# Performance work log

Measured on AMD Instinct MI355X. Metric: run time of the kernel, lower is better.

The kernel has to match this reference:

```python
import jax, jax.numpy as jnp
import numpy as np

N, E, C, H, EDGE_DIM, HID = 50000, 800000, 128, 8, 64, 512
D = C // H  # head dim = out_channels_conv


def layer_norm(x, g, b, eps=1e-5):
    mu = x.mean(-1, keepdims=True)
    var = ((x - mu) ** 2).mean(-1, keepdims=True)
    return (x - mu) * jax.lax.rsqrt(var + eps) * g + b


def _lin_init(k, fan_in, fan_out):
    s = 1.0 / np.sqrt(fan_in)
    kw, kb = jax.random.split(k)
    w = jax.random.uniform(kw, (fan_in, fan_out), minval=-s, maxval=s, dtype=jnp.float32)
    b = jax.random.uniform(kb, (fan_out,), minval=-s, maxval=s, dtype=jnp.float32)
    return w, b


def setup_inputs() -> dict:
    key = jax.random.key(0)
    ks = jax.random.split(key, 16)
    wq, bq = _lin_init(ks[0], C, C)
    wk, bk = _lin_init(ks[1], C, C)
    wv, bv = _lin_init(ks[2], C, C)
    ws, bs = _lin_init(ks[3], C, C)          # lin_self
    we, be = _lin_init(ks[4], EDGE_DIM, C)   # lin_edge
    wp, bp = _lin_init(ks[5], C, C)          # projection
    w1, b1 = _lin_init(ks[6], C, HID)        # node_dst_mlp[0]
    w2, b2 = _lin_init(ks[7], HID, C)        # node_dst_mlp[2]
    x = jax.random.normal(ks[8], (N, C), dtype=jnp.float32)
    edge_attr = jax.random.normal(ks[9], (E, EDGE_DIM), dtype=jnp.float32)
    edge_index = jax.random.randint(ks[10], (2, E), 0, N, dtype=jnp.int64)
    return dict(
        x=x, edge_attr=edge_attr, edge_index=edge_index,
        wq=wq, bq=bq, wk=wk, bk=bk, wv=wv, bv=bv, ws=ws, bs=bs,
        we=we, be=be, wp=wp, bp=bp, w1=w1, b1=b1, w2=w2, b2=b2,
        ln1_g=jnp.ones((C,), jnp.float32), ln1_b=jnp.zeros((C,), jnp.float32),
        ln2_g=jnp.ones((C,), jnp.float32), ln2_b=jnp.zeros((C,), jnp.float32),
    )


def reference(x, edge_attr, edge_index,
              wq, bq, wk, bk, wv, bv, ws, bs, we, be, wp, bp,
              w1, b1, w2, b2, ln1_g, ln1_b, ln2_g, ln2_b):
    src, dst = edge_index[0], edge_index[1]

    x_skip = x
    xn = layer_norm(x, ln1_g, ln1_b)                       # layer_norm_attention
    x_r = xn @ ws + bs                                     # lin_self residual
    q = (xn @ wq + bq).reshape(N, H, D)
    k = (xn @ wk + bk).reshape(N, H, D)
    v = (xn @ wv + bv).reshape(N, H, D)
    e = (edge_attr @ we + be).reshape(E, H, D)             # lin_edge (edge_pre_mlp = Identity)

    # edge-indexed multi-head attention: softmax over incoming edges per dst node
    ke = k[src] + e                                        # [E,H,D]
    alpha = jnp.einsum('ehd,ehd->eh', q[dst], ke) / np.sqrt(D)   # [E,H]
    amax = jax.lax.stop_gradient(jax.ops.segment_max(alpha, dst, num_segments=N))
    ex = jnp.exp(alpha - amax[dst])
    den = jax.ops.segment_sum(ex, dst, num_segments=N)
    w = ex / (den[dst] + 1e-16)                            # [E,H]
    out = jax.ops.segment_sum(w[:, :, None] * (v[src] + e), dst, num_segments=N)  # [N,H,D]
    out = out.reshape(N, C)

    out = (out + x_r) @ wp + bp                            # projection
    out = out + x_skip
    h = layer_norm(out, ln2_g, ln2_b)                      # layer_norm_mlp_dst
    h = jax.nn.gelu(h @ w1 + b1) @ w2 + b2                 # node_dst_mlp
    nodes_new = out + h
    return nodes_new, edge_attr
```

## Files before the change

kernel.cpp:

```cpp
#include <hip/hip_runtime.h>
#include <hip/hip_bf16.h>
#include <cstdio>

#define NN 50000
#define NE 800000
#define CC 128
#define EDIM 64
#define HIDN 512

using bf16 = __hip_bfloat16;
typedef short sh8 __attribute__((ext_vector_type(8)));
typedef float f32x4 __attribute__((ext_vector_type(4)));

static __device__ __forceinline__ float b2f(bf16 v){ return __bfloat162float(v); }
static __device__ __forceinline__ bf16 f2b(float v){ return __float2bfloat16(v); }
static __device__ __forceinline__ float u2f(unsigned short u){
    union { unsigned int i; float f; } w; w.i = ((unsigned int)u) << 16; return w.f;
}
static __device__ __forceinline__ unsigned short f2u(float f){
    bf16 b = __float2bfloat16(f);
    return *reinterpret_cast<unsigned short*>(&b);
}
static __device__ __forceinline__ float2 loadbf2(const bf16* p){
    __hip_bfloat162 v = *reinterpret_cast<const __hip_bfloat162*>(p);
    return make_float2(__bfloat162float(v.x), __bfloat162float(v.y));
}
static __device__ __forceinline__ float gelu_tanh(float x){
    const float c = 0.7978845608028654f;
    float u = c * (x + 0.044715f * x * x * x);
    return x / (1.0f + __expf(-2.0f * u));
}

constexpr size_t AL(size_t x){ return (x + 255) & ~(size_t)255; }
constexpr size_t OFF_FLAG = 0;
constexpr size_t OFF_DEG  = 256;
constexpr size_t OFF_ROW  = AL(OFF_DEG + (size_t)(NN + 1) * 4);
constexpr size_t OFF_CUR  = AL(OFF_ROW + (size_t)(NN + 1) * 4);
constexpr size_t OFF_EPOS = AL(OFF_CUR + (size_t)NN * 4);
constexpr size_t OFF_SRC  = AL(OFF_EPOS + (size_t)NE * 4);
constexpr size_t OFF_DST  = AL(OFF_SRC + (size_t)NE * 4);
constexpr size_t OFF_QC   = AL(OFF_DST + (size_t)NE * 4);
constexpr size_t OFF_KC   = AL(OFF_QC  + (size_t)NN * CC * 2);
constexpr size_t OFF_VC   = AL(OFF_KC  + (size_t)NN * CC * 2);
constexpr size_t OFF_ATT  = AL(OFF_VC  + (size_t)NN * CC * 2);
constexpr size_t OFF_PRM  = AL(OFF_ATT + (size_t)NN * CC * 2);
constexpr size_t PRM_ELEMS = 4*(16384+128) + 8192+128 + 16384+128 + 65536+512 + 65536+128 + 4*128;
constexpr size_t OFF_ALP  = AL(OFF_PRM + PRM_ELEMS * 2);
constexpr size_t OFF_VP   = AL(OFF_ALP + (size_t)NE * 8 * 4);
constexpr size_t OFF_XRC  = AL(OFF_VP + (size_t)NE * CC * 2);
constexpr size_t OFF_WFQ  = AL(OFF_XRC + (size_t)NN * CC * 2);
constexpr size_t OFF_WFK  = OFF_WFQ + 32768;
constexpr size_t OFF_WFV  = OFF_WFK + 32768;
constexpr size_t OFF_WFS  = OFF_WFV + 32768;
constexpr size_t OFF_WFP  = OFF_WFS + 32768;
constexpr size_t OFF_WF1  = OFF_WFP + 32768;
constexpr size_t OFF_WF2  = OFF_WF1 + 131072;
constexpr size_t OFF_WFE  = OFF_WF2 + 131072;
constexpr size_t OFF_BSUM = OFF_WFE + 16384;
constexpr size_t WS_NEED  = OFF_BSUM + 256;

__global__ void k_detect(const unsigned short* xw, const unsigned int* ew, int* flags){
    __shared__ int sw, sz;
    if (threadIdx.x == 0){ sw = 0; sz = 0; }
    __syncthreads();
    int w = 0;
    for (int i = threadIdx.x; i < 8192; i += 256){
        unsigned e = (xw[i] >> 7) & 0xFF;
        if (e == 0xFF || (e != 0 && (e < 0x60 || e > 0x90))) w++;
    }
    atomicAdd(&sw, w);
    int z = 0;
    for (int i = threadIdx.x; i < 2048; i += 256)
        if (ew[2*i+1] == 0u) z++;
    atomicAdd(&sz, z);
    __syncthreads();
    if (threadIdx.x == 0){
        flags[0] = (sw > 2048) ? 1 : 0;
        flags[1] = (sz > 1536) ? 1 : 0;
    }
}

struct CvtJob { const void* s; bf16* d; int n; };
struct CvtJobs { CvtJob j[20]; };
__global__ void k_cvt_all(CvtJobs jobs, const int* flags){
    const int f = flags[0];
    const int e = blockIdx.x >> 5;
    const CvtJob J = jobs.j[e];
    const int stride = 32 * 256;
    for (int i = (blockIdx.x & 31) * 256 + threadIdx.x; i < J.n; i += stride){
        if (f) J.d[i] = f2b(((const float*)J.s)[i]);
        else   J.d[i] = ((const bf16*)J.s)[i];
    }
}

__global__ void k_cvt_idx(const int* e32, int* srcI, int* dstI, int* deg, const int* flags){
    const int f = flags[1];
    int i = blockIdx.x * blockDim.x + threadIdx.x;
    const int stride = gridDim.x * blockDim.x;
    if (f){
        const long long* e64 = (const long long*)e32;
        for (; i < NE; i += stride){
            srcI[i] = (int)e64[i];
            const int d = (int)e64[NE + i];
            dstI[i] = d;
            atomicAdd(&deg[d], 1);
        }
    } else {
        for (; i < NE; i += stride){
            srcI[i] = e32[i];
            const int d = e32[NE + i];
            dstI[i] = d;
            atomicAdd(&deg[d], 1);
        }
    }
}

struct WJob { const bf16* W; bf16* WF; int K; int N; };
struct WJobs { WJob j[8]; };
__global__ void k_wprep_all(WJobs jobs){
    const WJob J = jobs.j[blockIdx.x / 48];
    const int KS = J.K >> 5;
    const int total = J.K * J.N;
    for (int o = (blockIdx.x % 48) * 256 + threadIdx.x; o < total; o += 48 * 256){
        const int j  = o & 7;
        const int ln = (o >> 3) & 63;
        const int tt = o >> 9;
        const int ks = tt % KS, ct = tt / KS;
        const int kk = (ks << 5) + ((ln >> 4) << 3) + j;
        const int c  = (ct << 4) + (ln & 15);
        J.WF[o] = J.W[kk * J.N + c];
    }
}

#define ASWZ(row, chunk)  (((row) << 8)  + ((((chunk) ^ ((row) & 15))) << 4))
#define HSWZ(row, chunk)  (((row) << 10) + ((((chunk) ^ ((row) & 15))) << 4))
#define EASWZ(row, chunk) (((row) << 7)  + ((((chunk) ^ ((row) & 7)))  << 4))

static __device__ __forceinline__ void gemm_nodes_128(
    const unsigned short* Abase, int row0, int lane,
    const bf16* __restrict__ WF, const bf16* __restrict__ bias,
    bf16* __restrict__ outp, int n0)
{
    const int rA = row0 + (lane & 15);
    sh8 af[4];
    #pragma unroll
    for (int ks = 0; ks < 4; ++ks)
        af[ks] = *(const sh8*)((const char*)Abase + ASWZ(rA, (ks << 2) + (lane >> 4)));
    f32x4 acc[8] = {};
    #pragma unroll
    for (int ks = 0; ks < 4; ++ks)
        #pragma unroll
        for (int ct = 0; ct < 8; ++ct){
            sh8 bfr = *(const sh8*)(WF + ((size_t)((ct << 2) + ks) * 64 + lane) * 8);
            acc[ct] = __builtin_amdgcn_mfma_f32_16x16x32_bf16(af[ks], bfr, acc[ct], 0, 0, 0);
        }
    #pragma unroll
    for (int ct = 0; ct < 8; ++ct){
        const int c = (ct << 4) + (lane & 15);
        const float bv = b2f(bias[c]);
        #pragma unroll
        for (int i = 0; i < 4; ++i){
            const int r = row0 + ((lane >> 4) << 2) + i;
            if (n0 + r < NN)
                outp[(size_t)(n0 + r) * CC + c] = f2b(acc[ct][i] + bv);
        }
    }
}

__global__ __launch_bounds__(256) void k_node_pre2(
    const void* __restrict__ x_raw, const int* __restrict__ flags,
    const bf16* __restrict__ WFq, const bf16* __restrict__ bq,
    const bf16* __restrict__ WFk, const bf16* __restrict__ bk,
    const bf16* __restrict__ WFv, const bf16* __restrict__ bv,
    const bf16* __restrict__ WFs, const bf16* __restrict__ bs,
    const bf16* __restrict__ g,  const bf16* __restrict__ bb,
    bf16* __restrict__ q, bf16* __restrict__ k, bf16* __restrict__ v,
    bf16* __restrict__ xr)
{
    __shared__ unsigned short A[64 * 128];
    const int t = threadIdx.x, lane = t & 63, wid = t >> 6;
    const int n0 = blockIdx.x * 64;

    if (flags[0]){
        const float* x = (const float*)x_raw;
        #pragma unroll
        for (int it = 0; it < 8; ++it){
            const int u = t + 256 * it;
            const int row = u >> 5, c = (u & 31) << 2;
            float4 a = make_float4(0.f, 0.f, 0.f, 0.f);
            if (n0 + row < NN)
                a = *(const float4*)&x[(size_t)(n0 + row) * CC + c];
            ushort4 b;
            b.x = f2u(a.x); b.y = f2u(a.y); b.z = f2u(a.z); b.w = f2u(a.w);
            *(ushort4*)((char*)A + ASWZ(row, c >> 3) + ((c & 7) << 1)) = b;
        }
    } else {
        const bf16* x = (const bf16*)x_raw;
        #pragma unroll
        for (int it = 0; it < 4; ++it){
            const int c8 = t + 256 * it;
            const int row = c8 >> 4, chunk = c8 & 15, col = chunk << 3;
            uint4 val = make_uint4(0u, 0u, 0u, 0u);
            if (n0 + row < NN)
                val = *(const uint4*)&x[(size_t)(n0 + row) * CC + col];
            *(uint4*)((char*)A + ASWZ(row, chunk)) = val;
        }
    }
    __syncthreads();

    {
        const int nd = wid * 16 + (lane & 15), qd = lane >> 4;
        float vals[32];
        #pragma unroll
        for (int i = 0; i < 4; ++i){
            uint4 u = *(const uint4*)((const char*)A + ASWZ(nd, (qd << 2) + i));
            unsigned uu[4] = {u.x, u.y, u.z, u.w};
            #pragma unroll
            for (int j2 = 0; j2 < 4; ++j2){
                vals[i*8 + j2*2]     = u2f((unsigned short)(uu[j2] & 0xFFFF));
                vals[i*8 + j2*2 + 1] = u2f((unsigned short)(uu[j2] >> 16));
            }
        }
        float s = 0.f;
        #pragma unroll
        for (int i = 0; i < 32; ++i) s += vals[i];
        s += __shfl_xor(s, 16); s += __shfl_xor(s, 32);
        const float mu = s * (1.0f / CC);
        float vv = 0.f;
        #pragma unroll
        for (int i = 0; i < 32; ++i){ const float d = vals[i] - mu; vv += d * d; }
        vv += __shfl_xor(vv, 16); vv += __shfl_xor(vv, 32);
        const float rstd = rsqrtf(vv * (1.0f / CC) + 1e-5f);
        #pragma unroll
        for (int i = 0; i < 4; ++i){
            unsigned w[4];
            #pragma unroll
            for (int j2 = 0; j2 < 4; ++j2){
                const int c0 = qd * 32 + i * 8 + j2 * 2;
                const float a0 = (vals[i*8+j2*2]   - mu) * rstd * b2f(g[c0])   + b2f(bb[c0]);
                const float a1 = (vals[i*8+j2*2+1] - mu) * rstd * b2f(g[c0+1]) + b2f(bb[c0+1]);
                w[j2] = (unsigned)f2u(a0) | ((unsigned)f2u(a1) << 16);
            }
            *(uint4*)((char*)A + ASWZ(nd, (qd << 2) + i)) = make_uint4(w[0], w[1], w[2], w[3]);
        }
    }
    __syncthreads();

    const int row0 = wid * 16;
    gemm_nodes_128(A, row0, lane, WFq, bq, q,  n0);
    gemm_nodes_128(A, row0, lane, WFk, bk, k,  n0);
    gemm_nodes_128(A, row0, lane, WFv, bv, v,  n0);
    gemm_nodes_128(A, row0, lane, WFs, bs, xr, n0);
}

__global__ __launch_bounds__(1024) void k_scan1(const int* __restrict__ deg,
                                                int* __restrict__ row, int* __restrict__ bsum){
    __shared__ int sb[1024];
    const int t = threadIdx.x;
    const int idx = blockIdx.x * 1024 + t;
    sb[t] = (idx < NN) ? deg[idx] : 0;
    __syncthreads();
    for (int off = 1; off < 1024; off <<= 1){
        int tv = (t >= off) ? sb[t - off] : 0;
        __syncthreads();
        sb[t] += tv;
        __syncthreads();
    }
    if (idx < NN) row[idx + 1] = sb[t];
    if (t == 1023) bsum[blockIdx.x] = sb[1023];
}

__global__ void k_scan2(int* __restrict__ bsum, int nb){
    int v = (threadIdx.x < nb) ? bsum[threadIdx.x] : 0;
    for (int off = 1; off < 64; off <<= 1){
        int u = __shfl_up(v, off);
        if (threadIdx.x >= off) v += u;
    }
    if (threadIdx.x < nb) bsum[threadIdx.x] = v;
}

__global__ __launch_bounds__(1024) void k_scan3(const int* __restrict__ bsum, int* __restrict__ row){
    const int idx = blockIdx.x * 1024 + threadIdx.x;
    const int add = (blockIdx.x > 0) ? bsum[blockIdx.x - 1] : 0;
    if (idx < NN) row[idx + 1] += add;
    if (idx == 0) row[0] = 0;
}

__global__ void k_scatter(const int* __restrict__ dst, const int* __restrict__ rowstart,
                          int* __restrict__ cursor, int* __restrict__ epos){
    const int i = blockIdx.x * blockDim.x + threadIdx.x;
    if (i < NE) {
        const int d = dst[i];
        const int p = atomicAdd(&cursor[d], 1);
        epos[i] = rowstart[d] + p;
    }
}

__global__ __launch_bounds__(256) void k_edge4(
    const void* __restrict__ ea_raw, const int* __restrict__ flags,
    const bf16* __restrict__ WFe, const bf16* __restrict__ be,
    const bf16* __restrict__ kv_q, const bf16* __restrict__ kv_k, const bf16* __restrict__ kv_v,
    const int* __restrict__ srcI, const int* __restrict__ dstI, const int* __restrict__ epos,
    float* __restrict__ alphap, unsigned short* __restrict__ vperm,
    void* __restrict__ outv)
{
    __shared__ unsigned short EA[64 * 64];
    __shared__ unsigned short ET[64 * 128];
    const int t = threadIdx.x, lane = t & 63, wid = t >> 6;
    const int e0 = blockIdx.x * 64;

    if (flags[0]){
        const float* ea = (const float*)ea_raw;
        float* outd = (float*)outv + (size_t)NN * CC;
        #pragma unroll
        for (int it = 0; it < 4; ++it){
            const int u = t + 256 * it;
            const int row = u >> 4, c = (u & 15) << 2;
            const size_t o = (size_t)(e0 + row) * EDIM + c;
            const float4 a = *(const float4*)&ea[o];
            *(float4*)&outd[o] = a;
            ushort4 b;
            b.x = f2u(a.x); b.y = f2u(a.y); b.z = f2u(a.z); b.w = f2u(a.w);
            *(ushort4*)((char*)EA + EASWZ(row, c >> 3) + ((c & 7) << 1)) = b;
        }
    } else {
        const unsigned short* ea = (const unsigned short*)ea_raw;
        unsigned short* outd = (unsigned short*)outv + (size_t)NN * CC;
        #pragma unroll
        for (int it = 0; it < 2; ++it){
            const int u = t + 256 * it;
            const int row = u >> 3, c = (u & 7) << 3;
            const size_t o = (size_t)(e0 + row) * EDIM + c;
            uint4 raw = *(const uint4*)&ea[o];
            *(uint4*)&outd[o] = raw;
            *(uint4*)((char*)EA + EASWZ(row, c >> 3)) = raw;
        }
    }
    __syncthreads();

    const int row0 = wid * 16;
    {
        const int rA = row0 + (lane & 15);
        sh8 af[2];
        #pragma unroll
        for (int ks = 0; ks < 2; ++ks)
            af[ks] = *(const sh8*)((const char*)EA + EASWZ(rA, (ks << 2) + (lane >> 4)));
        f32x4 acc[8] = {};
        #pragma unroll
        for (int ks = 0; ks < 2; ++ks)
            #pragma unroll
            for (int ct = 0; ct < 8; ++ct){
                sh8 bfr = *(const sh8*)(WFe + ((size_t)((ct << 1) + ks) * 64 + lane) * 8);
                acc[ct] = __builtin_amdgcn_mfma_f32_16x16x32_bf16(af[ks], bfr, acc[ct], 0, 0, 0);
            }
        #pragma unroll
        for (int ct = 0; ct < 8; ++ct){
            const int c = (ct << 4) + (lane & 15);
            const float bv = b2f(be[c]);
            #pragma unroll
            for (int i = 0; i < 4; ++i){
                const int r = row0 + ((lane >> 4) << 2) + i;
                *(unsigned short*)((char*)ET + ASWZ(r, c >> 3) + ((c & 7) << 1)) =
                    f2u(acc[ct][i] + bv);
            }
        }
    }
    __syncthreads();

    const int g = t >> 5, cT = t & 31, c = cT << 2;
    int s8[8], d8[8], p8[8];
    #pragma unroll
    for (int i = 0; i < 8; ++i){
        const int eid = e0 + g * 8 + i;
        s8[i] = srcI[eid];
        d8[i] = dstI[eid];
        p8[i] = epos[eid];
    }
    ushort4 kr[8], vr[8], qr[8];
    #pragma unroll
    for (int i = 0; i < 8; ++i) kr[i] = *(const ushort4*)&kv_k[(size_t)s8[i] * CC + c];
    #pragma unroll
    for (int i = 0; i < 8; ++i) vr[i] = *(const ushort4*)&kv_v[(size_t)s8[i] * CC + c];
    #pragma unroll
    for (int i = 0; i < 8; ++i) qr[i] = *(const ushort4*)&kv_q[(size_t)d8[i] * CC + c];
    #pragma unroll
    for (int i = 0; i < 8; ++i){
        const ushort4 ev = *(const ushort4*)((const char*)ET + ASWZ(g * 8 + i, c >> 3) + ((c & 7) << 1));
        const float e0_ = u2f(ev.x), e1_ = u2f(ev.y), e2_ = u2f(ev.z), e3_ = u2f(ev.w);
        float part = u2f(qr[i].x) * (e0_ + u2f(kr[i].x)) + u2f(qr[i].y) * (e1_ + u2f(kr[i].y))
                   + u2f(qr[i].z) * (e2_ + u2f(kr[i].z)) + u2f(qr[i].w) * (e3_ + u2f(kr[i].w));
        part += __shfl_xor(part, 1);
        part += __shfl_xor(part, 2);
        if ((cT & 3) == 0)
            alphap[(size_t)p8[i] * 8 + (cT >> 2)] = part * 0.25f;
        ushort4 vo;
        vo.x = f2u(e0_ + u2f(vr[i].x)); vo.y = f2u(e1_ + u2f(vr[i].y));
        vo.z = f2u(e2_ + u2f(vr[i].z)); vo.w = f2u(e3_ + u2f(vr[i].w));
        *(ushort4*)&vperm[(size_t)p8[i] * CC + c] = vo;
    }
}

__global__ __launch_bounds__(256) void k_attn3(
    const float* __restrict__ alphap, const bf16* __restrict__ vperm,
    const int* __restrict__ rowstart, bf16* __restrict__ attn_bf)
{
    const int t = threadIdx.x, lane = t & 63, wid = t >> 6;
    const int n = blockIdx.x * 4 + wid;
    const int h = lane >> 3;

    float m = -INFINITY, den = 0.0f;
    float2 num = make_float2(0.0f, 0.0f);

    const int jb = rowstart[n], je = rowstart[n + 1];
    for (int j = jb; j < je; ++j) {
        const float alpha = alphap[(size_t)j * 8 + h];
        const float2 v2 = loadbf2(&vperm[(size_t)j * CC + 2 * lane]);
        if (alpha > m) {
            const float sc = __expf(m - alpha);
            den *= sc; num.x *= sc; num.y *= sc;
            m = alpha;
        }
        const float p = __expf(alpha - m);
        den += p;
        num.x += p * v2.x;
        num.y += p * v2.y;
    }
    const float inv = 1.0f / (den + 1e-16f);
    __hip_bfloat162 pr;
    pr.x = f2b(num.x * inv);
    pr.y = f2b(num.y * inv);
    *reinterpret_cast<__hip_bfloat162*>(&attn_bf[(size_t)n * CC + 2 * lane]) = pr;
}

__global__ __launch_bounds__(256) void k_post2(
    const bf16* __restrict__ attn_bf, const bf16* __restrict__ xr,
    const void* __restrict__ x_raw,
    const bf16* __restrict__ WFp, const bf16* __restrict__ bp,
    const bf16* __restrict__ WF1, const bf16* __restrict__ b1,
    const bf16* __restrict__ WF2, const bf16* __restrict__ b2c,
    const bf16* __restrict__ g2, const bf16* __restrict__ bb2,
    void* __restrict__ outv, const int* __restrict__ flags)
{
    __shared__ unsigned short A[64 * 128];
    __shared__ unsigned short HID[64 * 512];
    const int t = threadIdx.x, lane = t & 63, wid = t >> 6;
    const int n0 = blockIdx.x * 64;
    const int f32io = flags[0];

    #pragma unroll
    for (int it = 0; it < 4; ++it){
        const int c8 = t + 256 * it;
        const int row = c8 >> 4, chunk = c8 & 15, col = chunk << 3;
        unsigned w[4] = {0u, 0u, 0u, 0u};
        if (n0 + row < NN){
            const size_t o = (size_t)(n0 + row) * CC + col;
            uint4 a4 = *(const uint4*)&attn_bf[o];
            uint4 r4 = *(const uint4*)&xr[o];
            unsigned au[4] = {a4.x, a4.y, a4.z, a4.w};
            unsigned ru[4] = {r4.x, r4.y, r4.z, r4.w};
            #pragma unroll
            for (int j2 = 0; j2 < 4; ++j2){
                const float lo = u2f((unsigned short)(au[j2] & 0xFFFF)) +
                                 u2f((unsigned short)(ru[j2] & 0xFFFF));
                const float hi = u2f((unsigned short)(au[j2] >> 16)) +
                                 u2f((unsigned short)(ru[j2] >> 16));
                w[j2] = (unsigned)f2u(lo) | ((unsigned)f2u(hi) << 16);
            }
        }
        *(uint4*)((char*)A + ASWZ(row, chunk)) = make_uint4(w[0], w[1], w[2], w[3]);
    }
    __syncthreads();

    const int row0 = wid * 16;
    const int rA = row0 + (lane & 15);

    float out2[8][4];
    {
        sh8 af[4];
        #pragma unroll
        for (int ks = 0; ks < 4; ++ks)
            af[ks] = *(const sh8*)((const char*)A + ASWZ(rA, (ks << 2) + (lane >> 4)));
        f32x4 acc[8] = {};
        #pragma unroll
        for (int ks = 0; ks < 4; ++ks)
            #pragma unroll
            for (int ct = 0; ct < 8; ++ct){
                sh8 bfr = *(const sh8*)(WFp + ((size_t)((ct << 2) + ks) * 64 + lane) * 8);
                acc[ct] = __builtin_amdgcn_mfma_f32_16x16x32_bf16(af[ks], bfr, acc[ct], 0, 0, 0);
            }
        #pragma unroll
        for (int ct = 0; ct < 8; ++ct){
            const int c = (ct << 4) + (lane & 15);
            const float bv = b2f(bp[c]);
            #pragma unroll
            for (int i = 0; i < 4; ++i){
                const int r = row0 + ((lane >> 4) << 2) + i;
                float xs = 0.f;
                if (n0 + r < NN){
                    const size_t o = (size_t)(n0 + r) * CC + c;
                    xs = f32io ? ((const float*)x_raw)[o] : b2f(((const bf16*)x_raw)[o]);
                }
                out2[ct][i] = acc[ct][i] + bv + xs;
            }
        }
    }

    {
        float mu[4], rstd[4];
        #pragma unroll
        for (int i = 0; i < 4; ++i){
            float s = 0.f;
            #pragma unroll
            for (int ct = 0; ct < 8; ++ct) s += out2[ct][i];
            s += __shfl_xor(s, 1); s += __shfl_xor(s, 2);
            s += __shfl_xor(s, 4); s += __shfl_xor(s, 8);
            mu[i] = s * (1.0f / CC);
        }
        #pragma unroll
        for (int i = 0; i < 4; ++i){
            float vv = 0.f;
            #pragma unroll
            for (int ct = 0; ct < 8; ++ct){ const float d = out2[ct][i] - mu[i]; vv += d * d; }
            vv += __shfl_xor(vv, 1); vv += __shfl_xor(vv, 2);
            vv += __shfl_xor(vv, 4); vv += __shfl_xor(vv, 8);
            rstd[i] = rsqrtf(vv * (1.0f / CC) + 1e-5f);
        }
        #pragma unroll
        for (int ct = 0; ct < 8; ++ct){
            const int c = (ct << 4) + (lane & 15);
            const float gv = b2f(g2[c]), bbv = b2f(bb2[c]);
            const int chunk = c >> 3;
            #pragma unroll
            for (int i = 0; i < 4; ++i){
                const int r = row0 + ((lane >> 4) << 2) + i;
                const float ln = (out2[ct][i] - mu[i]) * rstd[i] * gv + bbv;
                *(unsigned short*)((char*)A + ASWZ(r, chunk) + ((c & 7) << 1)) = f2u(ln);
            }
        }
    }

    {
        sh8 af[4];
        #pragma unroll
        for (int ks = 0; ks < 4; ++ks)
            af[ks] = *(const sh8*)((const char*)A + ASWZ(rA, (ks << 2) + (lane >> 4)));
        #pragma unroll
        for (int grp = 0; grp < 4; ++grp){
            f32x4 acc[8] = {};
            #pragma unroll
            for (int ks = 0; ks < 4; ++ks)
                #pragma unroll
                for (int ctl = 0; ctl < 8; ++ctl){
                    const int ct = grp * 8 + ctl;
                    sh8 bfr = *(const sh8*)(WF1 + ((size_t)((ct << 2) + ks) * 64 + lane) * 8);
                    acc[ctl] = __builtin_amdgcn_mfma_f32_16x16x32_bf16(af[ks], bfr, acc[ctl], 0, 0, 0);
                }
            #pragma unroll
            for (int ctl = 0; ctl < 8; ++ctl){
                const int ct = grp * 8 + ctl;
                const int c = (ct << 4) + (lane & 15);
                const float bv = b2f(b1[c]);
                const int chunk = c >> 3;
                #pragma unroll
                for (int i = 0; i < 4; ++i){
                    const int r = row0 + ((lane >> 4) << 2) + i;
                    const float h = gelu_tanh(acc[ctl][i] + bv);
                    *(unsigned short*)((char*)HID + HSWZ(r, chunk) + ((c & 7) << 1)) = f2u(h);
                }
            }
        }
    }

    {
        f32x4 acc[8] = {};
        #pragma unroll
        for (int ks = 0; ks < 16; ++ks){
            sh8 afh = *(const sh8*)((const char*)HID + HSWZ(rA, (ks << 2) + (lane >> 4)));
            #pragma unroll
            for (int ct = 0; ct < 8; ++ct){
                sh8 bfr = *(const sh8*)(WF2 + ((size_t)((ct << 4) + ks) * 64 + lane) * 8);
                acc[ct] = __builtin_amdgcn_mfma_f32_16x16x32_bf16(afh, bfr, acc[ct], 0, 0, 0);
            }
        }
        #pragma unroll
        for (int ct = 0; ct < 8; ++ct){
            const int c = (ct << 4) + (lane & 15);
            const float bv = b2f(b2c[c]);
            #pragma unroll
            for (int i = 0; i < 4; ++i){
                const int r = row0 + ((lane >> 4) << 2) + i;
                if (n0 + r < NN){
                    const float val = out2[ct][i] + acc[ct][i] + bv;
                    if (f32io) ((float*)outv)[(size_t)(n0 + r) * CC + c] = val;
                    else       ((bf16*)outv)[(size_t)(n0 + r) * CC + c] = f2b(val);
                }
            }
        }
    }
}

extern "C" void kernel_launch(void* const* d_in, const int* in_sizes, int n_in,
                              void* d_out, int out_size, void* d_ws, size_t ws_size,
                              hipStream_t stream)
{
    if (ws_size < WS_NEED) {
        fprintf(stderr, "[kl] WS TOO SMALL ws=%zu need=%zu\n", ws_size, WS_NEED);
        return;
    }

    char* ws = (char*)d_ws;
    int*  flags = (int*)(ws + OFF_FLAG);
    int*  deg   = (int*)(ws + OFF_DEG);
    int*  row   = (int*)(ws + OFF_ROW);
    int*  cur   = (int*)(ws + OFF_CUR);
    int*  epos  = (int*)(ws + OFF_EPOS);
    int*  srcI  = (int*)(ws + OFF_SRC);
    int*  dstI  = (int*)(ws + OFF_DST);
    int*  bsum  = (int*)(ws + OFF_BSUM);
    bf16* qC    = (bf16*)(ws + OFF_QC);
    bf16* kC    = (bf16*)(ws + OFF_KC);
    bf16* vC    = (bf16*)(ws + OFF_VC);
    bf16* attC  = (bf16*)(ws + OFF_ATT);
    bf16* xrC   = (bf16*)(ws + OFF_XRC);
    float* alphap = (float*)(ws + OFF_ALP);
    unsigned short* vperm = (unsigned short*)(ws + OFF_VP);
    bf16* WFq = (bf16*)(ws + OFF_WFQ);
    bf16* WFk = (bf16*)(ws + OFF_WFK);
    bf16* WFv = (bf16*)(ws + OFF_WFV);
    bf16* WFs = (bf16*)(ws + OFF_WFS);
    bf16* WFp = (bf16*)(ws + OFF_WFP);
    bf16* WF1 = (bf16*)(ws + OFF_WF1);
    bf16* WF2 = (bf16*)(ws + OFF_WF2);
    bf16* WFe = (bf16*)(ws + OFF_WFE);

    bf16* P = (bf16*)(ws + OFF_PRM);
    bf16 *wqC=P; P+=16384; bf16 *bqC=P; P+=128;
    bf16 *wkC=P; P+=16384; bf16 *bkC=P; P+=128;
    bf16 *wvC=P; P+=16384; bf16 *bvC=P; P+=128;
    bf16 *wsC=P; P+=16384; bf16 *bsC=P; P+=128;
    bf16 *weC=P; P+=8192;  bf16 *beC=P; P+=128;
    bf16 *wpC=P; P+=16384; bf16 *bpC=P; P+=128;
    bf16 *w1C=P; P+=65536; bf16 *b1C=P; P+=512;
    bf16 *w2C=P; P+=65536; bf16 *b2C=P; P+=128;
    bf16 *g1C=P; P+=128;   bf16 *n1C=P; P+=128;
    bf16 *g2C=P; P+=128;   bf16 *n2C=P; P+=128;

    hipMemsetAsync(deg, 0, (size_t)(NN + 1) * sizeof(int), stream);
    hipMemsetAsync(cur, 0, (size_t)NN * sizeof(int), stream);

    k_detect<<<1, 256, 0, stream>>>((const unsigned short*)d_in[0],
                                    (const unsigned int*)d_in[2], flags);

    {
        CvtJobs cj;
        bf16* dsts[20] = {wqC,bqC,wkC,bkC,wvC,bvC,wsC,bsC,weC,beC,
                          wpC,bpC,w1C,b1C,w2C,b2C,g1C,n1C,g2C,n2C};
        const int ns[20] = {16384,128,16384,128,16384,128,16384,128,8192,128,
                            16384,128,65536,512,65536,128,128,128,128,128};
        for (int i = 0; i < 20; ++i){ cj.j[i].s = d_in[3 + i]; cj.j[i].d = dsts[i]; cj.j[i].n = ns[i]; }
        k_cvt_all<<<20 * 32, 256, 0, stream>>>(cj, flags);
    }
    k_cvt_idx<<<1024, 256, 0, stream>>>((const int*)d_in[2], srcI, dstI, deg, flags);

    {
        WJobs wj;
        const WJob js[8] = {{wqC,WFq,128,128},{wkC,WFk,128,128},{wvC,WFv,128,128},
                            {wsC,WFs,128,128},{wpC,WFp,128,128},{w1C,WF1,128,512},
                            {w2C,WF2,512,128},{weC,WFe,64,128}};
        for (int i = 0; i < 8; ++i) wj.j[i] = js[i];
        k_wprep_all<<<8 * 48, 256, 0, stream>>>(wj);
    }

    const int NB64 = (NN + 63) / 64;
    const int NSC  = (NN + 1023) / 1024;
    k_node_pre2<<<NB64, 256, 0, stream>>>(d_in[0], flags, WFq, bqC, WFk, bkC, WFv, bvC,
                                          WFs, bsC, g1C, n1C, qC, kC, vC, xrC);
    k_scan1<<<NSC, 1024, 0, stream>>>(deg, row, bsum);
    k_scan2<<<1, 64, 0, stream>>>(bsum, NSC);
    k_scan3<<<NSC, 1024, 0, stream>>>(bsum, row);
    k_scatter<<<(NE + 255) / 256, 256, 0, stream>>>(dstI, row, cur, epos);
    k_edge4<<<NE / 64, 256, 0, stream>>>(d_in[1], flags, WFe, beC, qC, kC, vC,
                                         srcI, dstI, epos, alphap, vperm, d_out);
    k_attn3<<<NN / 4, 256, 0, stream>>>(alphap, (const bf16*)vperm, row, attC);
    k_post2<<<NB64, 256, 0, stream>>>(attC, xrC, d_in[0], WFp, bpC, WF1, b1C, WF2, b2C,
                                      g2C, n2C, d_out, flags);
}
```

Measured before the change: 537.4 us.

## Store attention logits in bf16, split MLP hidden buffer, fold scan2 into scan3

Attention logits are now written and read as bf16 instead of fp32, which halves that edge-sized traffic at some cost in precision. The post kernel computes the 512-wide hidden layer in two halves of 256 and accumulates the second GEMM per half. This halves the shared-memory HID buffer so more blocks can fit on a CU. The separate scan2 launch is removed and each scan3 block sums the preceding block totals itself, and the attention loop is unrolled by two so more loads are in flight.

```diff
diff --git a/kernel.cpp b/kernel.cpp
--- a/kernel.cpp
+++ b/kernel.cpp
@@ -46,7 +46,7 @@
 constexpr size_t OFF_PRM  = AL(OFF_ATT + (size_t)NN * CC * 2);
 constexpr size_t PRM_ELEMS = 4*(16384+128) + 8192+128 + 16384+128 + 65536+512 + 65536+128 + 4*128;
 constexpr size_t OFF_ALP  = AL(OFF_PRM + PRM_ELEMS * 2);
-constexpr size_t OFF_VP   = AL(OFF_ALP + (size_t)NE * 8 * 4);
+constexpr size_t OFF_VP   = AL(OFF_ALP + (size_t)NE * 8 * 2);
 constexpr size_t OFF_XRC  = AL(OFF_VP + (size_t)NE * CC * 2);
 constexpr size_t OFF_WFQ  = AL(OFF_XRC + (size_t)NN * CC * 2);
 constexpr size_t OFF_WFK  = OFF_WFQ + 32768;
@@ -133,7 +133,7 @@
 }
 
 #define ASWZ(row, chunk)  (((row) << 8)  + ((((chunk) ^ ((row) & 15))) << 4))
-#define HSWZ(row, chunk)  (((row) << 10) + ((((chunk) ^ ((row) & 15))) << 4))
+#define H2SWZ(row, chunk) (((row) << 9)  + ((((chunk) ^ ((row) & 15))) << 4))
 #define EASWZ(row, chunk) (((row) << 7)  + ((((chunk) ^ ((row) & 7)))  << 4))
 
 static __device__ __forceinline__ void gemm_nodes_128(
@@ -270,19 +270,18 @@
     if (t == 1023) bsum[blockIdx.x] = sb[1023];
 }
 
-__global__ void k_scan2(int* __restrict__ bsum, int nb){
-    int v = (threadIdx.x < nb) ? bsum[threadIdx.x] : 0;
-    for (int off = 1; off < 64; off <<= 1){
-        int u = __shfl_up(v, off);
-        if (threadIdx.x >= off) v += u;
-    }
-    if (threadIdx.x < nb) bsum[threadIdx.x] = v;
-}
-
 __global__ __launch_bounds__(1024) void k_scan3(const int* __restrict__ bsum, int* __restrict__ row){
-    const int idx = blockIdx.x * 1024 + threadIdx.x;
-    const int add = (blockIdx.x > 0) ? bsum[blockIdx.x - 1] : 0;
-    if (idx < NN) row[idx + 1] += add;
+    __shared__ int sadd;
+    const int t = threadIdx.x;
+    if (t < 64){
+        int a = 0;
+        for (int i = t; i < (int)blockIdx.x; i += 64) a += bsum[i];
+        for (int off = 32; off; off >>= 1) a += __shfl_xor(a, off);
+        if (t == 0) sadd = a;
+    }
+    __syncthreads();
+    const int idx = blockIdx.x * 1024 + t;
+    if (idx < NN) row[idx + 1] += sadd;
     if (idx == 0) row[0] = 0;
 }
 
@@ -301,7 +300,7 @@
     const bf16* __restrict__ WFe, const bf16* __restrict__ be,
     const bf16* __restrict__ kv_q, const bf16* __restrict__ kv_k, const bf16* __restrict__ kv_v,
     const int* __restrict__ srcI, const int* __restrict__ dstI, const int* __restrict__ epos,
-    float* __restrict__ alphap, unsigned short* __restrict__ vperm,
+    unsigned short* __restrict__ alphap, unsigned short* __restrict__ vperm,
     void* __restrict__ outv)
 {
     __shared__ unsigned short EA[64 * 64];
@@ -392,7 +391,7 @@
         part += __shfl_xor(part, 1);
         part += __shfl_xor(part, 2);
         if ((cT & 3) == 0)
-            alphap[(size_t)p8[i] * 8 + (cT >> 2)] = part * 0.25f;
+            alphap[(size_t)p8[i] * 8 + (cT >> 2)] = f2u(part * 0.25f);
         ushort4 vo;
         vo.x = f2u(e0_ + u2f(vr[i].x)); vo.y = f2u(e1_ + u2f(vr[i].y));
         vo.z = f2u(e2_ + u2f(vr[i].z)); vo.w = f2u(e3_ + u2f(vr[i].w));
@@ -401,7 +400,7 @@
 }
 
 __global__ __launch_bounds__(256) void k_attn3(
-    const float* __restrict__ alphap, const bf16* __restrict__ vperm,
+    const unsigned short* __restrict__ alphap, const bf16* __restrict__ vperm,
     const int* __restrict__ rowstart, bf16* __restrict__ attn_bf)
 {
     const int t = threadIdx.x, lane = t & 63, wid = t >> 6;
@@ -412,18 +411,37 @@
     float2 num = make_float2(0.0f, 0.0f);
 
     const int jb = rowstart[n], je = rowstart[n + 1];
-    for (int j = jb; j < je; ++j) {
-        const float alpha = alphap[(size_t)j * 8 + h];
-        const float2 v2 = loadbf2(&vperm[(size_t)j * CC + 2 * lane]);
-        if (alpha > m) {
-            const float sc = __expf(m - alpha);
+    int j = jb;
+    for (; j + 2 <= je; j += 2) {
+        const float a0 = u2f(alphap[(size_t)j * 8 + h]);
+        const float a1 = u2f(alphap[(size_t)(j + 1) * 8 + h]);
+        const float2 v0 = loadbf2(&vperm[(size_t)j * CC + 2 * lane]);
+        const float2 v1 = loadbf2(&vperm[(size_t)(j + 1) * CC + 2 * lane]);
+        if (a0 > m) {
+            const float sc = __expf(m - a0);
             den *= sc; num.x *= sc; num.y *= sc;
-            m = alpha;
-        }
-        const float p = __expf(alpha - m);
-        den += p;
-        num.x += p * v2.x;
-        num.y += p * v2.y;
+            m = a0;
+        }
+        const float p0 = __expf(a0 - m);
+        den += p0; num.x += p0 * v0.x; num.y += p0 * v0.y;
+        if (a1 > m) {
+            const float sc = __expf(m - a1);
+            den *= sc; num.x *= sc; num.y *= sc;
+            m = a1;
+        }
+        const float p1 = __expf(a1 - m);
+        den += p1; num.x += p1 * v1.x; num.y += p1 * v1.y;
+    }
+    if (j < je) {
+        const float a0 = u2f(alphap[(size_t)j * 8 + h]);
+        const float2 v0 = loadbf2(&vperm[(size_t)j * CC + 2 * lane]);
+        if (a0 > m) {
+            const float sc = __expf(m - a0);
+            den *= sc; num.x *= sc; num.y *= sc;
+            m = a0;
+        }
+        const float p0 = __expf(a0 - m);
+        den += p0; num.x += p0 * v0.x; num.y += p0 * v0.y;
     }
     const float inv = 1.0f / (den + 1e-16f);
     __hip_bfloat162 pr;
@@ -442,7 +460,7 @@
     void* __restrict__ outv, const int* __restrict__ flags)
 {
     __shared__ unsigned short A[64 * 128];
-    __shared__ unsigned short HID[64 * 512];
+    __shared__ unsigned short HID[64 * 256];
     const int t = threadIdx.x, lane = t & 63, wid = t >> 6;
     const int n0 = blockIdx.x * 64;
     const int f32io = flags[0];
@@ -544,42 +562,43 @@
         #pragma unroll
         for (int ks = 0; ks < 4; ++ks)
             af[ks] = *(const sh8*)((const char*)A + ASWZ(rA, (ks << 2) + (lane >> 4)));
-        #pragma unroll
-        for (int grp = 0; grp < 4; ++grp){
-            f32x4 acc[8] = {};
-            #pragma unroll
-            for (int ks = 0; ks < 4; ++ks)
+        f32x4 acc3[8] = {};
+        #pragma unroll
+        for (int hf = 0; hf < 2; ++hf){
+            #pragma unroll
+            for (int grp = 0; grp < 2; ++grp){
+                f32x4 acc[8] = {};
+                #pragma unroll
+                for (int ks = 0; ks < 4; ++ks)
+                    #pragma unroll
+                    for (int ctl = 0; ctl < 8; ++ctl){
+                        const int ct = hf * 16 + grp * 8 + ctl;
+                        sh8 bfr = *(const sh8*)(WF1 + ((size_t)((ct << 2) + ks) * 64 + lane) * 8);
+                        acc[ctl] = __builtin_amdgcn_mfma_f32_16x16x32_bf16(af[ks], bfr, acc[ctl], 0, 0, 0);
+                    }
                 #pragma unroll
                 for (int ctl = 0; ctl < 8; ++ctl){
-                    const int ct = grp * 8 + ctl;
-                    sh8 bfr = *(const sh8*)(WF1 + ((size_t)((ct << 2) + ks) * 64 + lane) * 8);
-                    acc[ctl] = __builtin_amdgcn_mfma_f32_16x16x32_bf16(af[ks], bfr, acc[ctl], 0, 0, 0);
+                    const int ct = hf * 16 + grp * 8 + ctl;
+                    const int c = (ct << 4) + (lane & 15);
+                    const int cl = c - (hf << 8);
+                    const float bv = b2f(b1[c]);
+                    const int chunk = cl >> 3;
+                    #pragma unroll
+                    for (int i = 0; i < 4; ++i){
+                        const int r = row0 + ((lane >> 4) << 2) + i;
+                        const float hh = gelu_tanh(acc[ctl][i] + bv);
+                        *(unsigned short*)((char*)HID + H2SWZ(r, chunk) + ((cl & 7) << 1)) = f2u(hh);
+                    }
                 }
-            #pragma unroll
-            for (int ctl = 0; ctl < 8; ++ctl){
-                const int ct = grp * 8 + ctl;
-                const int c = (ct << 4) + (lane & 15);
-                const float bv = b2f(b1[c]);
-                const int chunk = c >> 3;
+            }
+            #pragma unroll
+            for (int ks8 = 0; ks8 < 8; ++ks8){
+                sh8 afh = *(const sh8*)((const char*)HID + H2SWZ(rA, (ks8 << 2) + (lane >> 4)));
                 #pragma unroll
-                for (int i = 0; i < 4; ++i){
-                    const int r = row0 + ((lane >> 4) << 2) + i;
-                    const float h = gelu_tanh(acc[ctl][i] + bv);
-                    *(unsigned short*)((char*)HID + HSWZ(r, chunk) + ((c & 7) << 1)) = f2u(h);
+                for (int ct = 0; ct < 8; ++ct){
+                    sh8 bfr = *(const sh8*)(WF2 + ((size_t)((ct << 4) + (hf << 3) + ks8) * 64 + lane) * 8);
+                    acc3[ct] = __builtin_amdgcn_mfma_f32_16x16x32_bf16(afh, bfr, acc3[ct], 0, 0, 0);
                 }
-            }
-        }
-    }
-
-    {
-        f32x4 acc[8] = {};
-        #pragma unroll
-        for (int ks = 0; ks < 16; ++ks){
-            sh8 afh = *(const sh8*)((const char*)HID + HSWZ(rA, (ks << 2) + (lane >> 4)));
-            #pragma unroll
-            for (int ct = 0; ct < 8; ++ct){
-                sh8 bfr = *(const sh8*)(WF2 + ((size_t)((ct << 4) + ks) * 64 + lane) * 8);
-                acc[ct] = __builtin_amdgcn_mfma_f32_16x16x32_bf16(afh, bfr, acc[ct], 0, 0, 0);
             }
         }
         #pragma unroll
@@ -590,7 +609,7 @@
             for (int i = 0; i < 4; ++i){
                 const int r = row0 + ((lane >> 4) << 2) + i;
                 if (n0 + r < NN){
-                    const float val = out2[ct][i] + acc[ct][i] + bv;
+                    const float val = out2[ct][i] + acc3[ct][i] + bv;
                     if (f32io) ((float*)outv)[(size_t)(n0 + r) * CC + c] = val;
                     else       ((bf16*)outv)[(size_t)(n0 + r) * CC + c] = f2b(val);
                 }
@@ -622,8 +641,8 @@
     bf16* vC    = (bf16*)(ws + OFF_VC);
     bf16* attC  = (bf16*)(ws + OFF_ATT);
     bf16* xrC   = (bf16*)(ws + OFF_XRC);
-    float* alphap = (float*)(ws + OFF_ALP);
-    unsigned short* vperm = (unsigned short*)(ws + OFF_VP);
+    unsigned short* alphap = (unsigned short*)(ws + OFF_ALP);
+    unsigned short* vperm  = (unsigned short*)(ws + OFF_VP);
     bf16* WFq = (bf16*)(ws + OFF_WFQ);
     bf16* WFk = (bf16*)(ws + OFF_WFK);
     bf16* WFv = (bf16*)(ws + OFF_WFV);
@@ -676,7 +695,6 @@
     k_node_pre2<<<NB64, 256, 0, stream>>>(d_in[0], flags, WFq, bqC, WFk, bkC, WFv, bvC,
                                           WFs, bsC, g1C, n1C, qC, kC, vC, xrC);
     k_scan1<<<NSC, 1024, 0, stream>>>(deg, row, bsum);
-    k_scan2<<<1, 64, 0, stream>>>(bsum, NSC);
     k_scan3<<<NSC, 1024, 0, stream>>>(bsum, row);
     k_scatter<<<(NE + 255) / 256, 256, 0, stream>>>(dstI, row, cur, epos);
     k_edge4<<<NE / 64, 256, 0, stream>>>(d_in[1], flags, WFe, beC, qC, kC, vC,
```

New measurement: 549.6 us. +2.3%, slower.
